# Kernel optimization log

Measured on AMD Instinct MI355X. Metric: run time of the kernel, lower is better.

The kernel has to match this reference:

```python
import math
import jax, jax.numpy as jnp
import numpy as np

# Model hyperparameters (match init_kwargs)
LAYERS, BLOCKS = 10, 4
RC, DC, SC = 32, 32, 256          # residual / dilation / skip channels
CLASSES, L, K = 256, 1024, 3      # classes, input_length, kernel_size
B = 64                            # batch


def _dilations():
    """Replicates the (new_dilation, init_dilation) schedule built in __init__."""
    ds = []
    init = 1
    for _b in range(BLOCKS):
        d = 1
        for _i in range(LAYERS):
            ds.append((d, init))
            init = d
            d *= 2
    return ds


def dilate(x, dilation, init_dilation):
    """Faithful port of the torch dilate(): (n,c,l) -> (n*d/d0, c, l*d0/d)
    via permute/view/permute, zero-padding the start if l is not divisible."""
    n, c, l = x.shape
    if dilation == init_dilation:
        return x
    factor = dilation / init_dilation
    new_l = int(np.ceil(l / factor) * factor)
    if new_l != l:  # constant_pad_1d with pad_start=True
        x = jnp.pad(x, ((0, 0), (0, 0), (new_l - l, 0)))
        l = new_l
    l_new = int(math.ceil(l * init_dilation / dilation))
    n_new = int(math.ceil(n * dilation / init_dilation))
    x = jnp.transpose(x, (1, 2, 0)).reshape(c, l_new, n_new)  # (c, l, n) contiguous view
    return jnp.transpose(x, (2, 0, 1))


def conv1d(x, w, pad):
    # x: (N, Cin, L), w: (Cout, Cin, K)
    return jax.lax.conv_general_dilated(
        x, w, window_strides=(1,), padding=[(pad, pad)],
        dimension_numbers=("NCH", "OIH", "NCH"))


def setup_inputs() -> dict:
    key = jax.random.key(0)
    ks = jax.random.split(key, 8)
    NL = LAYERS * BLOCKS
    return {
        "input": jax.random.normal(ks[0], (B, 2, L), jnp.float32),
        "start_w": jax.random.normal(ks[1], (RC, 2, 1), jnp.float32) * 0.3,
        "filter_w": jax.random.normal(ks[2], (NL, DC, RC, K), jnp.float32) * 0.1,
        "gate_w": jax.random.normal(ks[3], (NL, DC, RC, K), jnp.float32) * 0.1,
        "res_w": jax.random.normal(ks[4], (NL, RC, DC, 1), jnp.float32) * 0.1,
        "skip_w": jax.random.normal(ks[5], (NL, SC, DC, 1), jnp.float32) * 0.1,
        "fc_w": jax.random.normal(ks[6], (CLASSES, SC * L), jnp.float32) * 0.002,
        "fc_b": jnp.zeros((CLASSES,), jnp.float32),
    }


def reference(input, start_w, filter_w, gate_w, res_w, skip_w, fc_w, fc_b):
    pad = K // 2
    x = conv1d(input, start_w, 0)  # (B, RC, L)
    skip = None
    for i, (d, d0) in enumerate(_dilations()):
        residual = dilate(x, d, d0)                              # fast-wavenet reshape
        f = jnp.tanh(conv1d(residual, filter_w[i], pad))
        g = jax.nn.sigmoid(conv1d(residual, gate_w[i], pad))
        x = f * g                                                # gated activation
        s = x if x.shape[2] == 1 else dilate(x, 1, d)            # undo dilation for skip
        s = conv1d(s, skip_w[i], 0)                              # (B, SC, L)
        skip = s if skip is None else s + skip[:, :, -s.shape[2]:]
        x = conv1d(x, res_w[i], 0) + residual                    # residual connection
    out = jax.nn.relu(skip.reshape(skip.shape[0], -1))           # (B, SC*L)
    return out @ fc_w.T + fc_b                                   # (B, CLASSES)
```

## Files before the change

kernel.cpp:

```cpp
#include <hip/hip_runtime.h>
#include <stdint.h>

typedef short bf16x8 __attribute__((ext_vector_type(8)));
typedef short s4 __attribute__((ext_vector_type(4)));
typedef float f32x4 __attribute__((ext_vector_type(4)));

#define NPOS 65536
#define MB (1024ull * 1024ull)
#define SK_PIECE 2097152

__device__ __forceinline__ unsigned short f32_bf16(float f) {
    union { float f; unsigned u; } v; v.f = f;
    unsigned u = v.u;
    u += 0x7fffu + ((u >> 16) & 1u);
    return (unsigned short)(u >> 16);
}

__device__ __forceinline__ s4 pk4_bf16(float a, float b, float c, float d) {
    union { unsigned u[2]; s4 v; } r;
    asm("v_cvt_pk_bf16_f32 %0, %1, %2" : "=v"(r.u[0]) : "v"(a), "v"(b));
    asm("v_cvt_pk_bf16_f32 %0, %1, %2" : "=v"(r.u[1]) : "v"(c), "v"(d));
    return r.v;
}

__device__ __forceinline__ bf16x8 pk8_bf16(const float* v) {
    union { unsigned u[4]; bf16x8 x; } r;
    asm("v_cvt_pk_bf16_f32 %0, %1, %2" : "=v"(r.u[0]) : "v"(v[0]), "v"(v[1]));
    asm("v_cvt_pk_bf16_f32 %0, %1, %2" : "=v"(r.u[1]) : "v"(v[2]), "v"(v[3]));
    asm("v_cvt_pk_bf16_f32 %0, %1, %2" : "=v"(r.u[2]) : "v"(v[4]), "v"(v[5]));
    asm("v_cvt_pk_bf16_f32 %0, %1, %2" : "=v"(r.u[3]) : "v"(v[6]), "v"(v[7]));
    return r.x;
}

__global__ void ws_probe_k(float* __restrict__ out, float mib) {
    int i = blockIdx.x * 256 + threadIdx.x;
    if (i < 16384) out[i] = mib;
}

__global__ void repack_fgw_k(const float* __restrict__ fw,
                             const float* __restrict__ gw,
                             unsigned short* __restrict__ out) {
    int idx = blockIdx.x * 256 + threadIdx.x;
    int ic = idx & 31;
    int r1 = idx >> 5;
    int rq = r1 & 63;
    int r2 = r1 >> 6;
    int k  = r2 % 3;
    int i  = r2 / 3;
    int part = rq >> 4;
    int m = rq & 15;
    int oc = ((m >> 2) << 3) + ((part & 1) << 2) + (m & 3);
    const float* src = (part < 2) ? fw : gw;
    out[idx] = f32_bf16(src[(((i * 32 + oc) * 32 + ic) * 3) + k]);
}

__global__ void repack_sw_k(const float* __restrict__ sw,
                            unsigned short* __restrict__ out) {
    int idx = blockIdx.x * 256 + threadIdx.x;
    out[idx] = f32_bf16(sw[idx]);
}

__global__ void repack_rw_k(const float* __restrict__ rw,
                            unsigned short* __restrict__ out) {
    int idx = blockIdx.x * 256 + threadIdx.x;
    int ic = idx & 31;
    int r1 = idx >> 5;
    int rq = r1 & 31;
    int i  = r1 >> 5;
    int rt = rq >> 4, m = rq & 15;
    int oc = ((m >> 2) << 3) + (rt << 2) + (m & 3);
    out[idx] = f32_bf16(rw[(i * 32 + oc) * 32 + ic]);
}

#define MFMA16(A, B, C) __builtin_amdgcn_mfma_f32_16x16x32_bf16(A, B, C, 0, 0, 0)

__global__ __launch_bounds__(1024, 4) void wavenet_rows_k(
    const float* __restrict__ in,
    const float* __restrict__ stw,
    const unsigned short* __restrict__ fgw_all,
    const unsigned short* __restrict__ rwb_all,
    unsigned short* __restrict__ xg_all)
{
    __shared__ __align__(16) unsigned short xb16[2][1024 * 32];
    const int tid = threadIdx.x;
    const int w = tid >> 6, lane = tid & 63;
    const int quad = lane >> 4, l15 = lane & 15;
    const int b = blockIdx.x;
    const f32x4 zero = {0.f, 0.f, 0.f, 0.f};

    float xreg[4][8];

    {
        float s0[8], s1[8];
#pragma unroll
        for (int j = 0; j < 8; ++j) {
            int c = quad * 8 + j;
            s0[j] = stw[c * 2 + 0];
            s1[j] = stw[c * 2 + 1];
        }
#pragma unroll
        for (int g = 0; g < 4; ++g) {
            int t = (w * 4 + g) * 16 + l15;
            float i0 = in[b * 2048 + t];
            float i1 = in[b * 2048 + 1024 + t];
#pragma unroll
            for (int j = 0; j < 8; ++j) xreg[g][j] = s0[j] * i0 + s1[j] * i1;
            *(bf16x8*)(xb16[0] + t * 32 + ((quad ^ (t & 3)) * 8)) = pk8_bf16(xreg[g]);
        }
    }
    __syncthreads();

#pragma unroll 1
    for (int i = 0; i < 40; ++i) {
        const int d = 1 << (i % 10);
        const unsigned short* fgw = fgw_all + (size_t)i * 6144;
        unsigned short* xg = xg_all + (size_t)i * ((size_t)NPOS * 32)
                                    + (size_t)b * (1024 * 32);
        const unsigned short* xcur = xb16[i & 1];
        unsigned short* xnxt = xb16[(i & 1) ^ 1];
        const bool dores = (i < 39);

        bf16x8 wf[3][2], wg[3][2];
#pragma unroll
        for (int k = 0; k < 3; ++k) {
            const unsigned short* wb = fgw + k * 2048;
#pragma unroll
            for (int mt = 0; mt < 2; ++mt) {
                wf[k][mt] = *(const bf16x8*)(wb + (mt * 16 + l15) * 32 + quad * 8);
                wg[k][mt] = *(const bf16x8*)(wb + ((mt + 2) * 16 + l15) * 32 + quad * 8);
            }
        }
        bf16x8 wr0, wr1;
        if (dores) {
            const unsigned short* rwb = rwb_all + (size_t)i * 1024;
            wr0 = *(const bf16x8*)(rwb + l15 * 32 + quad * 8);
            wr1 = *(const bf16x8*)(rwb + (16 + l15) * 32 + quad * 8);
        }

#pragma unroll
        for (int g = 0; g < 4; ++g) {
            const int tg = (w * 4 + g) * 16;
            const int tc = tg + l15;

            bf16x8 zz;
#pragma unroll
            for (int j = 0; j < 8; ++j) zz[j] = 0;

            f32x4 accf[2] = {zero, zero};
            f32x4 accg[2] = {zero, zero};
            {
                int ts = tc - d, tm = ts & 1023;
                bf16x8 rv = *(const bf16x8*)(xcur + tm * 32 + ((quad ^ (tm & 3)) * 8));
                bf16x8 b0 = (ts >= 0) ? rv : zz;
#pragma unroll
                for (int mt = 0; mt < 2; ++mt) {
                    accf[mt] = MFMA16(wf[0][mt], b0, accf[mt]);
                    accg[mt] = MFMA16(wg[0][mt], b0, accg[mt]);
                }
            }
            {
                bf16x8 b1 = *(const bf16x8*)(xcur + tc * 32 + ((quad ^ (tc & 3)) * 8));
#pragma unroll
                for (int mt = 0; mt < 2; ++mt) {
                    accf[mt] = MFMA16(wf[1][mt], b1, accf[mt]);
                    accg[mt] = MFMA16(wg[1][mt], b1, accg[mt]);
                }
            }
            {
                int ts = tc + d, tm = ts & 1023;
                bf16x8 rv = *(const bf16x8*)(xcur + tm * 32 + ((quad ^ (tm & 3)) * 8));
                bf16x8 b2 = (ts < 1024) ? rv : zz;
#pragma unroll
                for (int mt = 0; mt < 2; ++mt) {
                    accf[mt] = MFMA16(wf[2][mt], b2, accf[mt]);
                    accg[mt] = MFMA16(wg[2][mt], b2, accg[mt]);
                }
            }

            float gv[8];
#pragma unroll
            for (int mt = 0; mt < 2; ++mt)
#pragma unroll
                for (int r = 0; r < 4; ++r) {
                    float fv = accf[mt][r], gg = accg[mt][r];
                    fv = fminf(fmaxf(fv, -10.f), 10.f);
                    gg = fminf(fmaxf(gg, -15.f), 15.f);
                    float a = __expf(2.f * fv);
                    float c = __expf(-gg);
                    float rr = __builtin_amdgcn_rcpf((a + 1.f) * (1.f + c));
                    gv[mt * 4 + r] = (a - 1.f) * rr;
                }
            bf16x8 bx = pk8_bf16(gv);

            *(bf16x8*)(xg + (size_t)tc * 32 + quad * 8) = bx;

            if (dores) {
                f32x4 a0 = MFMA16(wr0, bx, zero);
                f32x4 a1 = MFMA16(wr1, bx, zero);
#pragma unroll
                for (int r = 0; r < 4; ++r) {
                    xreg[g][r]     += a0[r];
                    xreg[g][4 + r] += a1[r];
                }
            }
        }

        if (dores) {
#pragma unroll
            for (int g = 0; g < 4; ++g) {
                int t = (w * 4 + g) * 16 + l15;
                *(bf16x8*)(xnxt + t * 32 + ((quad ^ (t & 3)) * 8)) = pk8_bf16(xreg[g]);
            }
        }
        __syncthreads();
    }
}

__global__ __launch_bounds__(256) void skip_gemm_k(
    const unsigned short* __restrict__ xg_all,
    const unsigned short* __restrict__ swb,
    unsigned short* __restrict__ sk)
{
    __shared__ __align__(16) unsigned short lds[256 * 72];
    int tid = threadIdx.x;
    int w = tid >> 6, lane = tid & 63;
    int quad = lane >> 4, l15 = lane & 15;
    int p0 = blockIdx.x * 64;
    f32x4 zero = {0.f, 0.f, 0.f, 0.f};
    f32x4 acc[4][4];
#pragma unroll
    for (int a = 0; a < 4; ++a)
#pragma unroll
        for (int c = 0; c < 4; ++c) acc[a][c] = zero;

    const unsigned short* bbase = xg_all + ((size_t)(p0 + l15)) * 32 + quad * 8;
    const unsigned short* abase = swb + ((size_t)(w * 64 + l15)) * 32 + quad * 8;

    bf16x8 bcur[4], acur[4], bnxt[4], anxt[4];
#pragma unroll
    for (int ct = 0; ct < 4; ++ct) bcur[ct] = *(const bf16x8*)(bbase + ct * 512);
#pragma unroll
    for (int rt = 0; rt < 4; ++rt) acur[rt] = *(const bf16x8*)(abase + rt * 512);

#pragma unroll 2
    for (int i = 0; i < 40; ++i) {
        if (i < 39) {
            const unsigned short* bn = bbase + (size_t)(i + 1) * NPOS * 32;
            const unsigned short* an = abase + (size_t)(i + 1) * 8192;
#pragma unroll
            for (int ct = 0; ct < 4; ++ct) bnxt[ct] = *(const bf16x8*)(bn + ct * 512);
#pragma unroll
            for (int rt = 0; rt < 4; ++rt) anxt[rt] = *(const bf16x8*)(an + rt * 512);
        }
#pragma unroll
        for (int rt = 0; rt < 4; ++rt)
#pragma unroll
            for (int ct = 0; ct < 4; ++ct)
                acc[rt][ct] = __builtin_amdgcn_mfma_f32_16x16x32_bf16(acur[rt], bcur[ct], acc[rt][ct], 0, 0, 0);
#pragma unroll
        for (int ct = 0; ct < 4; ++ct) bcur[ct] = bnxt[ct];
#pragma unroll
        for (int rt = 0; rt < 4; ++rt) acur[rt] = anxt[rt];
    }

#pragma unroll
    for (int rt = 0; rt < 4; ++rt)
#pragma unroll
        for (int ct = 0; ct < 4; ++ct)
#pragma unroll
            for (int r = 0; r < 4; ++r) {
                float v = acc[rt][ct][r];
                v = v > 0.f ? v : 0.f;
                lds[(w * 64 + rt * 16 + quad * 4 + r) * 72 + ct * 16 + l15] = f32_bf16(v);
            }
    __syncthreads();
    {
        size_t pbbase = (size_t)(p0 >> 6) * 2048;
#pragma unroll
        for (int j = 0; j < 8; ++j) {
            int idx = tid + 256 * j;
            int sc = idx >> 3, tc = idx & 7;
            int4 v = *(const int4*)(lds + sc * 72 + tc * 8);
            unsigned short* dst = sk + (size_t)(sc >> 5) * SK_PIECE + pbbase
                                     + (sc & 31) * 64 + tc * 8;
            *(int4*)dst = v;
        }
    }
}

__global__ __launch_bounds__(256) void fc_part_k(
    const unsigned short* __restrict__ sk,
    const float* __restrict__ fw,
    float* __restrict__ part)
{
    __shared__ __align__(16) unsigned short blds[2][256 * 32];
    int tid = threadIdx.x;
    int w = tid >> 6, lane = tid & 63;
    int quad = lane >> 4, l15 = lane & 15;
    int kb = blockIdx.x;
    int sc = kb >> 1;
    int tbase = (kb & 1) * 512;
    f32x4 zero = {0.f, 0.f, 0.f, 0.f};
    f32x4 acc[4][4];
#pragma unroll
    for (int a = 0; a < 4; ++a)
#pragma unroll
        for (int c = 0; c < 4; ++c) acc[a][c] = zero;

    const unsigned short* skp = sk + (size_t)(sc >> 5) * SK_PIECE + (sc & 31) * 64;
    const int cls_s = tid >> 3, kc_s = tid & 7;
    const float* fwbase = fw + (size_t)cls_s * 262144 + sc * 1024 + tbase + kc_s * 4;

    auto stage = [&](int it, int buf) {
        float4 v[8];
#pragma unroll
        for (int jj = 0; jj < 8; ++jj)
            v[jj] = *(const float4*)(fwbase + (size_t)jj * 32 * 262144 + it * 32);
#pragma unroll
        for (int jj = 0; jj < 8; ++jj) {
            int cls = cls_s + jj * 32;
            int slot = (kc_s >> 1) ^ (cls & 3);
            *(s4*)(blds[buf] + cls * 32 + slot * 8 + (kc_s & 1) * 4) =
                pk4_bf16(v[jj].x, v[jj].y, v[jj].z, v[jj].w);
        }
    };

    stage(0, 0);
    __syncthreads();
    for (int it = 0; it < 16; ++it) {
        int buf = it & 1;
        if (it < 15) stage(it + 1, buf ^ 1);
        int t = tbase + it * 32 + quad * 8;
        bf16x8 af[4];
#pragma unroll
        for (int rt = 0; rt < 4; ++rt) {
            int bi = rt * 16 + l15;
            af[rt] = *(const bf16x8*)(skp + (size_t)(bi * 16 + (t >> 6)) * 2048 + (t & 63));
        }
#pragma unroll
        for (int ct = 0; ct < 4; ++ct) {
            int cls = w * 64 + ct * 16 + l15;
            bf16x8 bw = *(const bf16x8*)(blds[buf] + cls * 32 + ((quad ^ (cls & 3)) * 8));
#pragma unroll
            for (int rt = 0; rt < 4; ++rt)
                acc[rt][ct] = __builtin_amdgcn_mfma_f32_16x16x32_bf16(af[rt], bw, acc[rt][ct], 0, 0, 0);
        }
        __syncthreads();
    }
#pragma unroll
    for (int rt = 0; rt < 4; ++rt)
#pragma unroll
        for (int ct = 0; ct < 4; ++ct)
#pragma unroll
            for (int r = 0; r < 4; ++r) {
                int bb = rt * 16 + quad * 4 + r;
                int cls = w * 64 + ct * 16 + l15;
                part[((size_t)kb * 64 + bb) * 256 + cls] = acc[rt][ct][r];
            }
}

__global__ void fc_r1_k(const float* __restrict__ part, float* __restrict__ part2) {
    int blk = blockIdx.x;
    int b = blk & 63, kc = blk >> 6;
    int cls = threadIdx.x;
    float s = 0.f;
    for (int kb = kc * 64; kb < kc * 64 + 64; ++kb)
        s += part[((size_t)kb * 64 + b) * 256 + cls];
    part2[((size_t)kc * 64 + b) * 256 + cls] = s;
}

__global__ void fc_r2_k(const float* __restrict__ part2,
                        const float* __restrict__ fb,
                        float* __restrict__ out) {
    int b = blockIdx.x, cls = threadIdx.x;
    float s = fb[cls];
    for (int kc = 0; kc < 8; ++kc)
        s += part2[((size_t)kc * 64 + b) * 256 + cls];
    out[b * 256 + cls] = s;
}

extern "C" void kernel_launch(void* const* d_in, const int* in_sizes, int n_in,
                              void* d_out, int out_size, void* d_ws, size_t ws_size,
                              hipStream_t stream) {
    const float* input    = (const float*)d_in[0];
    const float* start_w  = (const float*)d_in[1];
    const float* filter_w = (const float*)d_in[2];
    const float* gate_w   = (const float*)d_in[3];
    const float* res_w    = (const float*)d_in[4];
    const float* skip_w   = (const float*)d_in[5];
    const float* fc_w     = (const float*)d_in[6];
    const float* fc_b     = (const float*)d_in[7];
    float* out = (float*)d_out;

    const size_t REQUIRED = 192 * MB;
    if (ws_size < REQUIRED) {
        ws_probe_k<<<64, 256, 0, stream>>>(out, (float)(ws_size >> 20));
        return;
    }

    char* ws = (char*)d_ws;
    unsigned short* xg_all = (unsigned short*)(ws);
    unsigned short* sk     = (unsigned short*)(ws);
    float*          part   = (float*)(ws + 32 * MB);
    float*          part2  = (float*)(ws + 64 * MB);
    unsigned short* fgw    = (unsigned short*)(ws + 176 * MB);
    unsigned short* swb    = (unsigned short*)(ws + 176 * MB + 512 * 1024);
    unsigned short* rwb    = (unsigned short*)(ws + 178 * MB);

    repack_fgw_k<<<960, 256, 0, stream>>>(filter_w, gate_w, fgw);
    repack_sw_k<<<1280, 256, 0, stream>>>(skip_w, swb);
    repack_rw_k<<<160, 256, 0, stream>>>(res_w, rwb);

    wavenet_rows_k<<<64, 1024, 0, stream>>>(input, start_w, fgw, rwb, xg_all);

    skip_gemm_k<<<1024, 256, 0, stream>>>(xg_all, swb, sk);
    fc_part_k<<<512, 256, 0, stream>>>(sk, fc_w, part);
    fc_r1_k<<<512, 256, 0, stream>>>(part, part2);
    fc_r2_k<<<64, 256, 0, stream>>>(part2, fc_b, out);
}
```

Before: 837.4 us.

## Halve wavenet block threads with single LDS buffer; stage skip GEMM via global_load_lds

The per-sample wavenet kernel now runs 512 threads per block, each wave covering 8 time groups instead of 4. It uses one LDS activation buffer instead of two, with an extra barrier before the residual write-back so all reads finish first. The skip GEMM now streams its activation tiles into double-buffered LDS with direct global-to-LDS loads, swizzled to avoid bank conflicts, and remaps block indices to spread position tiles. This is meant to cut register and LDS pressure and improve memory access patterns. The price is less parallelism per sample in the serial 40-layer loop and an extra sync per layer.

```diff
diff --git a/kernel.cpp b/kernel.cpp
--- a/kernel.cpp
+++ b/kernel.cpp
@@ -74,21 +74,21 @@
 
 #define MFMA16(A, B, C) __builtin_amdgcn_mfma_f32_16x16x32_bf16(A, B, C, 0, 0, 0)
 
-__global__ __launch_bounds__(1024, 4) void wavenet_rows_k(
+__global__ __launch_bounds__(512, 4) void wavenet_rows_k(
     const float* __restrict__ in,
     const float* __restrict__ stw,
     const unsigned short* __restrict__ fgw_all,
     const unsigned short* __restrict__ rwb_all,
     unsigned short* __restrict__ xg_all)
 {
-    __shared__ __align__(16) unsigned short xb16[2][1024 * 32];
+    __shared__ __align__(16) unsigned short xb16[1024 * 32];
     const int tid = threadIdx.x;
     const int w = tid >> 6, lane = tid & 63;
     const int quad = lane >> 4, l15 = lane & 15;
     const int b = blockIdx.x;
     const f32x4 zero = {0.f, 0.f, 0.f, 0.f};
 
-    float xreg[4][8];
+    float xreg[8][8];
 
     {
         float s0[8], s1[8];
@@ -99,13 +99,13 @@
             s1[j] = stw[c * 2 + 1];
         }
 #pragma unroll
-        for (int g = 0; g < 4; ++g) {
-            int t = (w * 4 + g) * 16 + l15;
+        for (int g = 0; g < 8; ++g) {
+            int t = (w * 8 + g) * 16 + l15;
             float i0 = in[b * 2048 + t];
             float i1 = in[b * 2048 + 1024 + t];
 #pragma unroll
             for (int j = 0; j < 8; ++j) xreg[g][j] = s0[j] * i0 + s1[j] * i1;
-            *(bf16x8*)(xb16[0] + t * 32 + ((quad ^ (t & 3)) * 8)) = pk8_bf16(xreg[g]);
+            *(bf16x8*)(xb16 + t * 32 + ((quad ^ (t & 3)) * 8)) = pk8_bf16(xreg[g]);
         }
     }
     __syncthreads();
@@ -116,8 +116,6 @@
         const unsigned short* fgw = fgw_all + (size_t)i * 6144;
         unsigned short* xg = xg_all + (size_t)i * ((size_t)NPOS * 32)
                                     + (size_t)b * (1024 * 32);
-        const unsigned short* xcur = xb16[i & 1];
-        unsigned short* xnxt = xb16[(i & 1) ^ 1];
         const bool dores = (i < 39);
 
         bf16x8 wf[3][2], wg[3][2];
@@ -138,9 +136,8 @@
         }
 
 #pragma unroll
-        for (int g = 0; g < 4; ++g) {
-            const int tg = (w * 4 + g) * 16;
-            const int tc = tg + l15;
+        for (int g = 0; g < 8; ++g) {
+            const int tc = (w * 8 + g) * 16 + l15;
 
             bf16x8 zz;
 #pragma unroll
@@ -150,7 +147,7 @@
             f32x4 accg[2] = {zero, zero};
             {
                 int ts = tc - d, tm = ts & 1023;
-                bf16x8 rv = *(const bf16x8*)(xcur + tm * 32 + ((quad ^ (tm & 3)) * 8));
+                bf16x8 rv = *(const bf16x8*)(xb16 + tm * 32 + ((quad ^ (tm & 3)) * 8));
                 bf16x8 b0 = (ts >= 0) ? rv : zz;
 #pragma unroll
                 for (int mt = 0; mt < 2; ++mt) {
@@ -159,7 +156,7 @@
                 }
             }
             {
-                bf16x8 b1 = *(const bf16x8*)(xcur + tc * 32 + ((quad ^ (tc & 3)) * 8));
+                bf16x8 b1 = *(const bf16x8*)(xb16 + tc * 32 + ((quad ^ (tc & 3)) * 8));
 #pragma unroll
                 for (int mt = 0; mt < 2; ++mt) {
                     accf[mt] = MFMA16(wf[1][mt], b1, accf[mt]);
@@ -168,7 +165,7 @@
             }
             {
                 int ts = tc + d, tm = ts & 1023;
-                bf16x8 rv = *(const bf16x8*)(xcur + tm * 32 + ((quad ^ (tm & 3)) * 8));
+                bf16x8 rv = *(const bf16x8*)(xb16 + tm * 32 + ((quad ^ (tm & 3)) * 8));
                 bf16x8 b2 = (ts < 1024) ? rv : zz;
 #pragma unroll
                 for (int mt = 0; mt < 2; ++mt) {
@@ -206,13 +203,14 @@
         }
 
         if (dores) {
-#pragma unroll
-            for (int g = 0; g < 4; ++g) {
-                int t = (w * 4 + g) * 16 + l15;
-                *(bf16x8*)(xnxt + t * 32 + ((quad ^ (t & 3)) * 8)) = pk8_bf16(xreg[g]);
-            }
-        }
-        __syncthreads();
+            __syncthreads();
+#pragma unroll
+            for (int g = 0; g < 8; ++g) {
+                int t = (w * 8 + g) * 16 + l15;
+                *(bf16x8*)(xb16 + t * 32 + ((quad ^ (t & 3)) * 8)) = pk8_bf16(xreg[g]);
+            }
+            __syncthreads();
+        }
     }
 }
 
@@ -225,7 +223,8 @@
     int tid = threadIdx.x;
     int w = tid >> 6, lane = tid & 63;
     int quad = lane >> 4, l15 = lane & 15;
-    int p0 = blockIdx.x * 64;
+    int pb = (blockIdx.x & 7) * 128 + (blockIdx.x >> 3);
+    int p0 = pb * 64;
     f32x4 zero = {0.f, 0.f, 0.f, 0.f};
     f32x4 acc[4][4];
 #pragma unroll
@@ -233,36 +232,53 @@
 #pragma unroll
         for (int c = 0; c < 4; ++c) acc[a][c] = zero;
 
-    const unsigned short* bbase = xg_all + ((size_t)(p0 + l15)) * 32 + quad * 8;
+    const int gswz = tid ^ ((tid >> 3) & 7);
+    int rslot[4];
+#pragma unroll
+    for (int ct = 0; ct < 4; ++ct) {
+        int u = (ct * 16 + l15) * 4 + quad;
+        rslot[ct] = u ^ ((u >> 3) & 7);
+    }
+
     const unsigned short* abase = swb + ((size_t)(w * 64 + l15)) * 32 + quad * 8;
 
-    bf16x8 bcur[4], acur[4], bnxt[4], anxt[4];
-#pragma unroll
-    for (int ct = 0; ct < 4; ++ct) bcur[ct] = *(const bf16x8*)(bbase + ct * 512);
+    auto stage = [&](int i, int s) {
+        const unsigned short* g = xg_all + ((size_t)i * NPOS + p0) * 32 + gswz * 8;
+        unsigned short* l = lds + s * 2048 + w * 512;
+        __builtin_amdgcn_global_load_lds(
+            (const __attribute__((address_space(1))) unsigned int*)g,
+            (__attribute__((address_space(3))) unsigned int*)l, 16, 0, 0);
+    };
+
+    stage(0, 0);
+    bf16x8 acur[4], anxt[4];
 #pragma unroll
     for (int rt = 0; rt < 4; ++rt) acur[rt] = *(const bf16x8*)(abase + rt * 512);
 
 #pragma unroll 2
     for (int i = 0; i < 40; ++i) {
-        if (i < 39) {
-            const unsigned short* bn = bbase + (size_t)(i + 1) * NPOS * 32;
+        int cb = i & 1;
+        __syncthreads();
+        if (i + 1 < 40) {
+            stage(i + 1, cb ^ 1);
             const unsigned short* an = abase + (size_t)(i + 1) * 8192;
 #pragma unroll
-            for (int ct = 0; ct < 4; ++ct) bnxt[ct] = *(const bf16x8*)(bn + ct * 512);
-#pragma unroll
             for (int rt = 0; rt < 4; ++rt) anxt[rt] = *(const bf16x8*)(an + rt * 512);
         }
+        const unsigned short* bufc = lds + cb * 2048;
+        bf16x8 bfr[4];
+#pragma unroll
+        for (int ct = 0; ct < 4; ++ct) bfr[ct] = *(const bf16x8*)(bufc + rslot[ct] * 8);
 #pragma unroll
         for (int rt = 0; rt < 4; ++rt)
 #pragma unroll
             for (int ct = 0; ct < 4; ++ct)
-                acc[rt][ct] = __builtin_amdgcn_mfma_f32_16x16x32_bf16(acur[rt], bcur[ct], acc[rt][ct], 0, 0, 0);
-#pragma unroll
-        for (int ct = 0; ct < 4; ++ct) bcur[ct] = bnxt[ct];
+                acc[rt][ct] = MFMA16(acur[rt], bfr[ct], acc[rt][ct]);
 #pragma unroll
         for (int rt = 0; rt < 4; ++rt) acur[rt] = anxt[rt];
     }
 
+    __syncthreads();
 #pragma unroll
     for (int rt = 0; rt < 4; ++rt)
 #pragma unroll
@@ -275,7 +291,7 @@
             }
     __syncthreads();
     {
-        size_t pbbase = (size_t)(p0 >> 6) * 2048;
+        size_t pbbase = (size_t)pb * 2048;
 #pragma unroll
         for (int j = 0; j < 8; ++j) {
             int idx = tid + 256 * j;
@@ -343,7 +359,7 @@
             bf16x8 bw = *(const bf16x8*)(blds[buf] + cls * 32 + ((quad ^ (cls & 3)) * 8));
 #pragma unroll
             for (int rt = 0; rt < 4; ++rt)
-                acc[rt][ct] = __builtin_amdgcn_mfma_f32_16x16x32_bf16(af[rt], bw, acc[rt][ct], 0, 0, 0);
+                acc[rt][ct] = MFMA16(af[rt], bw, acc[rt][ct]);
         }
         __syncthreads();
     }
@@ -411,7 +427,7 @@
     repack_sw_k<<<1280, 256, 0, stream>>>(skip_w, swb);
     repack_rw_k<<<160, 256, 0, stream>>>(res_w, rwb);
 
-    wavenet_rows_k<<<64, 1024, 0, stream>>>(input, start_w, fgw, rwb, xg_all);
+    wavenet_rows_k<<<64, 512, 0, stream>>>(input, start_w, fgw, rwb, xg_all);
 
     skip_gemm_k<<<1024, 256, 0, stream>>>(xg_all, swb, sk);
     fc_part_k<<<512, 256, 0, stream>>>(sk, fc_w, part);
```

Measured after the change: 1.025 ms. 1.22x slower.
